# Performance work log

Hardware: AMD Instinct MI355X
Metric: run time of the kernel (lower is better)

The kernel has to match this reference:

```python
import jax, jax.numpy as jnp
import numpy as np

K = 3       # attractive nearest neighbors
J = 3       # repulsive offset (uses dist[:, :, J:])
ALPHA = 0.1
NU = 1e-3


def setup_inputs() -> dict:
    key = jax.random.key(0)
    k1, k2 = jax.random.split(key, 2)
    phi_p = jax.random.normal(k1, (4, 512, 64, 64), dtype=jnp.float32)
    memory_bank = jax.random.normal(k2, (16384, 512), dtype=jnp.float32)
    r = jnp.ones((1,), dtype=jnp.float32)
    return {"phi_p": phi_p, "memory_bank": memory_bank, "r": r}


def reference(phi_p, memory_bank, r):
    B, C, H, W = phi_p.shape
    # b c h w -> b (h w) c
    x = phi_p.reshape(B, C, H * W).transpose(0, 2, 1)
    x2 = jnp.sum(x * x, axis=-1, keepdims=True)            # [B, HW, 1]
    m2 = jnp.sum(memory_bank * memory_bank, axis=-1)       # [N]
    d2 = x2 + m2[None, None, :] - 2.0 * jnp.einsum('bnc,mc->bnm', x, memory_bank)
    d2 = jnp.maximum(d2, 0.0)                              # [B, HW, N]
    # smallest K+J squared distances, ascending (topk(largest=False))
    neg_top, _ = jax.lax.top_k(-d2, K + J)
    dist = -neg_top                                        # [B, HW, K+J]
    r2 = r ** 2
    scores_att = dist[:, :, :K] - r2
    loss_att = jnp.mean(jnp.maximum(scores_att, 0.0)) / NU
    scores_rep = r2 - dist[:, :, J:] - ALPHA
    loss_rep = jnp.mean(jnp.maximum(scores_rep, 0.0)) / NU
    return loss_att + loss_rep
```

## Files before the change

### kernel.cpp

```cpp
#include <hip/hip_runtime.h>
#include <cfloat>

#define B_   4
#define C_   512
#define HW_  4096
#define R_   16384
#define N_   16384
#define ALPHA_ 0.1f
#define SCALE_ ((float)(1000.0/49152.0))

typedef unsigned int u32;
typedef unsigned short u16;
typedef unsigned char u8;
typedef __attribute__((ext_vector_type(2))) unsigned long long u64x2;
typedef __attribute__((ext_vector_type(4))) float f32x4;

typedef const __attribute__((address_space(1))) u32* gas_u32;
typedef __attribute__((address_space(3))) u32* las_u32;

__device__ __forceinline__ void async16(const void* g, void* l) {
    __builtin_amdgcn_global_load_lds((gas_u32)g, (las_u32)l, 16, 0, 0);
}

__device__ __forceinline__ u32 pk_fp8x4(float a, float b, float c, float d) {
    u32 v = __builtin_amdgcn_cvt_pk_fp8_f32(a, b, 0, false);
    v = __builtin_amdgcn_cvt_pk_fp8_f32(c, d, v, true);
    return v;
}

__device__ __forceinline__ void ins6(float (&t)[6], float v) {
    if (v < t[5]) {
        t[5] = v;
        #pragma unroll
        for (int q = 5; q >= 1; --q) {
            float lo = fminf(t[q-1], t[q]);
            float hi = fmaxf(t[q-1], t[q]);
            t[q-1] = lo; t[q] = hi;
        }
    }
}

__global__ void conv_mem_kernel(const float* __restrict__ mem,
                                u8* __restrict__ Mb, float* __restrict__ m2) {
    int w = threadIdx.x >> 6, l = threadIdx.x & 63;
    int row = blockIdx.x * 4 + w;
    const float4* p = (const float4*)(mem + (size_t)row * C_);
    float4 a = p[l], b = p[l + 64];
    float s = a.x*a.x + a.y*a.y + a.z*a.z + a.w*a.w
            + b.x*b.x + b.y*b.y + b.z*b.z + b.w*b.w;
    *(u32*)(Mb + (size_t)row * C_ + l*4)       = pk_fp8x4(a.x, a.y, a.z, a.w);
    *(u32*)(Mb + (size_t)row * C_ + 256 + l*4) = pk_fp8x4(b.x, b.y, b.z, b.w);
    #pragma unroll
    for (int off = 32; off > 0; off >>= 1) s += __shfl_down(s, off);
    if (l == 0) m2[row] = s;
}

__global__ void conv_phi_kernel(const float* __restrict__ phi, u8* __restrict__ Xb,
                                float* __restrict__ x2) {
    __shared__ float T[64][65];
    int t = threadIdx.x;
    int n0 = blockIdx.x * 64, c0 = blockIdx.y * 64, b = blockIdx.z;
    const float* src = phi + ((size_t)b * C_ + c0) * HW_ + n0;
    int l = t & 63, cg = t >> 6;
    float sq = 0.f;
    #pragma unroll
    for (int p = 0; p < 16; ++p) {
        int c = cg + p * 4;
        float v = src[(size_t)c * HW_ + l];
        T[c][l] = v;
        sq = fmaf(v, v, sq);
    }
    atomicAdd(&x2[(size_t)b * HW_ + n0 + l], sq);
    __syncthreads();
    int cq = t & 15, gl0 = t >> 4;
    #pragma unroll
    for (int p = 0; p < 4; ++p) {
        int gl = gl0 + p * 16;
        u32 v = pk_fp8x4(T[cq*4+0][gl], T[cq*4+1][gl],
                         T[cq*4+2][gl], T[cq*4+3][gl]);
        size_t g = (size_t)b * HW_ + n0 + gl;
        *(u32*)(Xb + g * C_ + c0 + cq*4) = v;
    }
}

template<int NC>
__global__ __launch_bounds__(256, 3) void gemm_topk_kernel(
    const u8* __restrict__ Xb, const u8* __restrict__ Mb,
    const float* __restrict__ m2, float* __restrict__ P ) {
    __shared__ __align__(16) u8 smem[32768];
    const int t = threadIdx.x;
    const int w = t >> 6, l = t & 63;
    const int id   = blockIdx.x;
    const int xcd  = id & 7;
    const int cy   = (xcd * NC) >> 3;
    const int xsub = xcd - cy * (8 / NC);
    const int bx   = (id >> 3) + xsub * (256 * NC / 8);
    const int g0  = bx * 64;
    const int n0c = cy * (N_ / NC);
    const int mband = w * 32;
    const int fm  = l & 15;
    const int rq  = l >> 4;
    const int pc  = (rq ^ ((fm >> 1) & 3)) * 16;
    const int srow4 = l >> 2;
    const int soff  = (((l & 3) ^ ((l >> 3) & 3)) * 16);

    u64x2 ax[4][2];
    {
        const u8* Xr = Xb + (size_t)(g0 + w*16 + fm) * C_ + rq * 16;
        #pragma unroll
        for (int s = 0; s < 4; ++s) {
            ax[s][0] = *(const u64x2*)(Xr + s*128);
            ax[s][1] = *(const u64x2*)(Xr + s*128 + 64);
        }
    }

    float top[4][6];
    #pragma unroll
    for (int s4 = 0; s4 < 4; ++s4)
        #pragma unroll
        for (int q = 0; q < 6; ++q) top[s4][q] = FLT_MAX;

    {
        const u8* Msrc = Mb + (size_t)(n0c + mband) * C_;
        #pragma unroll
        for (int h = 0; h < 2; ++h)
            #pragma unroll
            for (int i = 0; i < 2; ++i)
                async16(Msrc + (size_t)(i*16 + srow4) * C_ + h*64 + soff,
                        smem + mband*64 + h*8192 + i*1024);
    }
    __syncthreads();

    const int NT = N_ / NC / 128;
    #pragma unroll 1
    for (int nt = 0; nt < NT; ++nt) {
        const int n0 = n0c + nt * 128;

        f32x4 acc[8];
        #pragma unroll
        for (int n = 0; n < 8; ++n) acc[n] = (f32x4)0.f;

        #pragma unroll
        for (int s = 0; s < 4; ++s) {
            {
                const int nt2 = (s == 3) ? nt + 1 : nt;
                const int s2  = (s + 1) & 3;
                if (nt2 < NT) {
                    const u8* Msrc = Mb + (size_t)(n0c + nt2*128 + mband) * C_ + s2*128;
                    u8* dst = smem + ((s+1)&1)*16384 + mband*64;
                    #pragma unroll
                    for (int h = 0; h < 2; ++h)
                        #pragma unroll
                        for (int i = 0; i < 2; ++i)
                            async16(Msrc + (size_t)(i*16 + srow4) * C_ + h*64 + soff,
                                    dst + h*8192 + i*1024);
                }
            }
            const u8* bufp = smem + (s&1)*16384;
            #pragma unroll
            for (int h = 0; h < 2; ++h) {
                const u8* Mh = bufp + h * 8192;
                const u64x2 a = ax[s][h];
                #pragma unroll
                for (int n = 0; n < 8; ++n) {
                    u64x2 bv = *(const u64x2*)(Mh + (n*16 + fm) * 64 + pc);
                    acc[n] = __builtin_amdgcn_mfma_f32_16x16x32_fp8_fp8(
                        (long)a.x, (long)bv.x, acc[n], 0, 0, 0);
                    acc[n] = __builtin_amdgcn_mfma_f32_16x16x32_fp8_fp8(
                        (long)a.y, (long)bv.y, acc[n], 0, 0, 0);
                }
            }

            if (s == 3) {
                float m2w[8];
                #pragma unroll
                for (int n = 0; n < 8; ++n) m2w[n] = m2[n0 + n * 16 + fm];
                #pragma unroll
                for (int j = 0; j < 4; ++j) {
                    float d0 = m2w[0] - 2.f * acc[0][j];
                    float d1 = m2w[1] - 2.f * acc[1][j];
                    float d2 = m2w[2] - 2.f * acc[2][j];
                    float d3 = m2w[3] - 2.f * acc[3][j];
                    float d4 = m2w[4] - 2.f * acc[4][j];
                    float d5 = m2w[5] - 2.f * acc[5][j];
                    float d6 = m2w[6] - 2.f * acc[6][j];
                    float d7 = m2w[7] - 2.f * acc[7][j];
                    float vmin = fminf(fminf(fminf(d0, d1), fminf(d2, d3)),
                                       fminf(fminf(d4, d5), fminf(d6, d7)));
                    float (&tt)[6] = top[j];
                    if (vmin < tt[5]) {
                        ins6(tt, d0); ins6(tt, d1); ins6(tt, d2); ins6(tt, d3);
                        ins6(tt, d4); ins6(tt, d5); ins6(tt, d6); ins6(tt, d7);
                    }
                }
            }
            __syncthreads();
        }
    }

    float* Mg = (float*)smem;
    #pragma unroll
    for (int j = 0; j < 4; ++j) {
        int lrow = w * 16 + rq * 4 + j;
        #pragma unroll
        for (int q = 0; q < 6; ++q)
            Mg[lrow * 97 + fm * 6 + q] = top[j][q];
    }
    __syncthreads();
    if (t < 64) {
        float t6[6];
        #pragma unroll
        for (int q = 0; q < 6; ++q) t6[q] = FLT_MAX;
        const float* row = Mg + t * 97;
        for (int v = 0; v < 96; ++v) ins6(t6, row[v]);
        float* dst = P + ((size_t)(g0 + t) * NC + cy) * 6;
        #pragma unroll
        for (int q = 0; q < 6; ++q) dst[q] = t6[q];
    }
}

template<int NC>
__global__ void finalize_kernel(const float* __restrict__ P, const float* __restrict__ x2,
                                const float* __restrict__ rp, float* __restrict__ out) {
    int g = blockIdx.x * 256 + threadIdx.x;
    float t6[6];
    #pragma unroll
    for (int q = 0; q < 6; ++q) t6[q] = FLT_MAX;
    const f32x4* pp = (const f32x4*)(P + (size_t)g * (NC * 6));
    #pragma unroll
    for (int q = 0; q < NC * 6 / 4; ++q) {
        f32x4 v = pp[q];
        ins6(t6, v.x); ins6(t6, v.y); ins6(t6, v.z); ins6(t6, v.w);
    }
    float x2g = x2[g];
    float rv = rp[0], r2 = rv * rv;
    float s = 0.f;
    #pragma unroll
    for (int i = 0; i < 3; ++i) {
        float d = fmaxf(t6[i] + x2g, 0.f);
        s += fmaxf(d - r2, 0.f);
    }
    #pragma unroll
    for (int i = 3; i < 6; ++i) {
        float d = fmaxf(t6[i] + x2g, 0.f);
        s += fmaxf(r2 - d - ALPHA_, 0.f);
    }
    #pragma unroll
    for (int off = 32; off > 0; off >>= 1) s += __shfl_down(s, off);
    __shared__ float red[4];
    int w = threadIdx.x >> 6, l = threadIdx.x & 63;
    if (l == 0) red[w] = s;
    __syncthreads();
    if (threadIdx.x == 0)
        atomicAdd(out, (red[0] + red[1] + red[2] + red[3]) * SCALE_);
}

#define TM 64
#define TN 64
#define KC 64
#define LDP 68

__global__ void m2_kernel(const float* __restrict__ mem, float* __restrict__ m2) {
    int wave = threadIdx.x >> 6, lane = threadIdx.x & 63;
    int row = blockIdx.x * 4 + wave;
    const float4* p = reinterpret_cast<const float4*>(mem + (size_t)row * C_);
    float4 a = p[lane], b = p[lane + 64];
    float s = a.x*a.x + a.y*a.y + a.z*a.z + a.w*a.w
            + b.x*b.x + b.y*b.y + b.z*b.z + b.w*b.w;
    #pragma unroll
    for (int off = 32; off > 0; off >>= 1) s += __shfl_down(s, off);
    if (lane == 0) m2[row] = s;
}

__global__ void x2f_kernel(const float* __restrict__ phi, float* __restrict__ x2) {
    int g = blockIdx.x * blockDim.x + threadIdx.x;
    int b = g >> 12;
    int n = g & 4095;
    const float* p = phi + (size_t)b * C_ * HW_ + n;
    float s = 0.f;
    #pragma unroll 8
    for (int c = 0; c < C_; ++c) {
        float v = p[(size_t)c * HW_];
        s = fmaf(v, v, s);
    }
    x2[g] = s;
}

__global__ __launch_bounds__(256) void dist_loss_kernel(
    const float* __restrict__ phi, const float* __restrict__ mem,
    const float* __restrict__ rp,  const float* __restrict__ m2,
    const float* __restrict__ x2,  float* __restrict__ out) {
    __shared__ float smem[2 * TM * LDP];
    float* xs = smem;
    float* ms = smem + TM * LDP;
    const int tid = threadIdx.x;
    const int tx = tid & 15, ty = tid >> 4;
    const int g0 = blockIdx.x * TM;
    const int b = g0 >> 12, n0img = g0 & 4095;
    const float* phiB = phi + (size_t)b * C_ * HW_ + n0img;
    float top[4][6];
    #pragma unroll
    for (int i = 0; i < 4; ++i)
        #pragma unroll
        for (int q = 0; q < 6; ++q) top[i][q] = FLT_MAX;
    float x2v[4];
    #pragma unroll
    for (int i = 0; i < 4; ++i) x2v[i] = x2[g0 + ty * 4 + i];
    for (int nt = 0; nt < N_ / TN; ++nt) {
        const int n0 = nt * TN;
        float acc[4][4];
        #pragma unroll
        for (int i = 0; i < 4; ++i)
            #pragma unroll
            for (int j = 0; j < 4; ++j) acc[i][j] = 0.f;
        for (int s = 0; s < C_ / KC; ++s) {
            const int k0 = s * KC;
            {
                int rr = tid & 63, cb = tid >> 6;
                #pragma unroll
                for (int p = 0; p < 16; ++p) {
                    int cc = p * 4 + cb;
                    xs[rr * LDP + cc] = phiB[(size_t)(k0 + cc) * HW_ + rr];
                }
            }
            {
                int kq = tid & 15, cb = tid >> 4;
                #pragma unroll
                for (int p = 0; p < 4; ++p) {
                    int c = p * 16 + cb;
                    float4 v = *reinterpret_cast<const float4*>(
                        mem + (size_t)(n0 + c) * C_ + k0 + kq * 4);
                    ms[(kq*4+0)*LDP + c] = v.x; ms[(kq*4+1)*LDP + c] = v.y;
                    ms[(kq*4+2)*LDP + c] = v.z; ms[(kq*4+3)*LDP + c] = v.w;
                }
            }
            __syncthreads();
            #pragma unroll
            for (int kq = 0; kq < KC / 4; ++kq) {
                float4 xa[4], mb[4];
                #pragma unroll
                for (int i = 0; i < 4; ++i)
                    xa[i] = *reinterpret_cast<const float4*>(&xs[(ty*4+i)*LDP + kq*4]);
                #pragma unroll
                for (int kk = 0; kk < 4; ++kk)
                    mb[kk] = *reinterpret_cast<const float4*>(&ms[(kq*4+kk)*LDP + tx*4]);
                #pragma unroll
                for (int i = 0; i < 4; ++i) {
                    const float xk[4] = {xa[i].x, xa[i].y, xa[i].z, xa[i].w};
                    #pragma unroll
                    for (int kk = 0; kk < 4; ++kk) {
                        const float mc[4] = {mb[kk].x, mb[kk].y, mb[kk].z, mb[kk].w};
                        #pragma unroll
                        for (int j = 0; j < 4; ++j)
                            acc[i][j] = fmaf(xk[kk], mc[j], acc[i][j]);
                    }
                }
            }
            __syncthreads();
        }
        #pragma unroll
        for (int j = 0; j < 4; ++j) {
            float m2v = m2[n0 + tx * 4 + j];
            #pragma unroll
            for (int i = 0; i < 4; ++i) {
                float d = fmaxf(x2v[i] + m2v - 2.f * acc[i][j], 0.f);
                ins6(top[i], d);
            }
        }
    }
    __syncthreads();
    float* mg = smem;
    #pragma unroll
    for (int i = 0; i < 4; ++i)
        #pragma unroll
        for (int q = 0; q < 6; ++q)
            mg[(ty*4+i)*97 + tx*6 + q] = top[i][q];
    __syncthreads();
    if (tid < 64) {
        float t6[6];
        #pragma unroll
        for (int q = 0; q < 6; ++q) t6[q] = FLT_MAX;
        const float* row = mg + tid * 97;
        for (int v = 0; v < 96; ++v) ins6(t6, row[v]);
        float rv = rp[0], r2 = rv * rv;
        float s = fmaxf(t6[0]-r2,0.f) + fmaxf(t6[1]-r2,0.f) + fmaxf(t6[2]-r2,0.f)
                + fmaxf(r2-t6[3]-ALPHA_,0.f) + fmaxf(r2-t6[4]-ALPHA_,0.f)
                + fmaxf(r2-t6[5]-ALPHA_,0.f);
        #pragma unroll
        for (int off = 32; off > 0; off >>= 1) s += __shfl_down(s, off);
        if (tid == 0) atomicAdd(out, s * SCALE_);
    }
}

extern "C" void kernel_launch(void* const* d_in, const int* in_sizes, int n_in,
                              void* d_out, int out_size, void* d_ws, size_t ws_size,
                              hipStream_t stream) {
    const float* phi = (const float*)d_in[0];
    const float* mem = (const float*)d_in[1];
    const float* rp  = (const float*)d_in[2];
    float* out = (float*)d_out;

    const size_t offX  = 0;
    const size_t offM  = (size_t)R_ * C_;
    const size_t offx2 = offM + (size_t)N_ * C_;
    const size_t offm2 = offx2 + (size_t)R_ * 4;
    const size_t offP  = offm2 + (size_t)N_ * 4;
    const size_t need4 = offP + (size_t)R_ * 4 * 6 * 4;

    hipMemsetAsync(out, 0, sizeof(float), stream);

    if (ws_size >= need4) {
        u8*    Xb = (u8*)((char*)d_ws + offX);
        u8*    Mb = (u8*)((char*)d_ws + offM);
        float* x2 = (float*)((char*)d_ws + offx2);
        float* m2 = (float*)((char*)d_ws + offm2);
        float* P  = (float*)((char*)d_ws + offP);

        hipMemsetAsync(x2, 0, (size_t)R_ * 4, stream);
        conv_mem_kernel<<<N_ / 4, 256, 0, stream>>>(mem, Mb, m2);
        conv_phi_kernel<<<dim3(HW_ / 64, C_ / 64, B_), 256, 0, stream>>>(phi, Xb, x2);
        gemm_topk_kernel<4><<<dim3(256 * 4, 1), 256, 0, stream>>>(Xb, Mb, m2, P);
        finalize_kernel<4><<<R_ / 256, 256, 0, stream>>>(P, x2, rp, out);
    } else {
        float* m2 = (float*)d_ws;
        float* x2 = m2 + N_;
        m2_kernel<<<N_ / 4, 256, 0, stream>>>(mem, m2);
        x2f_kernel<<<R_ / 256, 256, 0, stream>>>(phi, x2);
        dist_loss_kernel<<<R_ / TM, 256, 0, stream>>>(phi, mem, rp, m2, x2, out);
    }
}
```

Baseline: 346.2 us.

## Triple-buffer memory-bank tiles in 64-byte stages and stage m2 in LDS

Replaces the double-buffered 128-column K stages with a three-slot rotating ring of 64-column stages, prefetching two stages ahead and synchronising with a partial vmcnt wait plus a single barrier per stage. The m2 norms for the block's column range are loaded once into shared memory asynchronously instead of being read from global memory every tile. This is meant to hide global-load latency and cut barrier stalls, at the cost of more LDS per block (which may reduce occupancy) and twice as many barriers per tile. The wrap-around prefetch issues redundant loads at the end, which are drained before the final reduction.

```diff
diff --git a/kernel.cpp b/kernel.cpp
--- a/kernel.cpp
+++ b/kernel.cpp
@@ -87,7 +87,7 @@
 __global__ __launch_bounds__(256, 3) void gemm_topk_kernel(
     const u8* __restrict__ Xb, const u8* __restrict__ Mb,
     const float* __restrict__ m2, float* __restrict__ P ) {
-    __shared__ __align__(16) u8 smem[32768];
+    __shared__ __align__(16) u8 smem[40960];
     const int t = threadIdx.x;
     const int w = t >> 6, l = t & 63;
     const int id   = blockIdx.x;
@@ -120,61 +120,62 @@
         #pragma unroll
         for (int q = 0; q < 6; ++q) top[s4][q] = FLT_MAX;
 
+    float* m2s = (float*)(smem + 24576);
     {
-        const u8* Msrc = Mb + (size_t)(n0c + mband) * C_;
-        #pragma unroll
-        for (int h = 0; h < 2; ++h)
-            #pragma unroll
-            for (int i = 0; i < 2; ++i)
-                async16(Msrc + (size_t)(i*16 + srow4) * C_ + h*64 + soff,
-                        smem + mband*64 + h*8192 + i*1024);
-    }
-    __syncthreads();
-
+        const float* src = m2 + n0c + (w * 4) * 256 + l * 4;
+        u8* dst = smem + 24576 + (w * 4) * 1024;
+        #pragma unroll
+        for (int i = 0; i < 4; ++i)
+            async16(src + i * 256, dst + i * 1024);
+    }
+    {
+        #pragma unroll
+        for (int i = 0; i < 2; ++i)
+            async16(Mb + (size_t)(n0c + mband + i*16 + srow4) * C_ + 0 + soff,
+                    smem + mband*64 + i*1024);
+        #pragma unroll
+        for (int i = 0; i < 2; ++i)
+            async16(Mb + (size_t)(n0c + mband + i*16 + srow4) * C_ + 64 + soff,
+                    smem + 8192 + mband*64 + i*1024);
+    }
+
+    u8 *q0 = smem, *q1 = smem + 8192, *q2 = smem + 16384;
     const int NT = N_ / NC / 128;
     #pragma unroll 1
     for (int nt = 0; nt < NT; ++nt) {
-        const int n0 = n0c + nt * 128;
-
         f32x4 acc[8];
         #pragma unroll
         for (int n = 0; n < 8; ++n) acc[n] = (f32x4)0.f;
 
         #pragma unroll
-        for (int s = 0; s < 4; ++s) {
+        for (int ss = 0; ss < 8; ++ss) {
+            asm volatile("s_waitcnt vmcnt(2)" ::: "memory");
+            __builtin_amdgcn_s_barrier();
             {
-                const int nt2 = (s == 3) ? nt + 1 : nt;
-                const int s2  = (s + 1) & 3;
-                if (nt2 < NT) {
-                    const u8* Msrc = Mb + (size_t)(n0c + nt2*128 + mband) * C_ + s2*128;
-                    u8* dst = smem + ((s+1)&1)*16384 + mband*64;
-                    #pragma unroll
-                    for (int h = 0; h < 2; ++h)
-                        #pragma unroll
-                        for (int i = 0; i < 2; ++i)
-                            async16(Msrc + (size_t)(i*16 + srow4) * C_ + h*64 + soff,
-                                    dst + h*8192 + i*1024);
-                }
-            }
-            const u8* bufp = smem + (s&1)*16384;
-            #pragma unroll
-            for (int h = 0; h < 2; ++h) {
-                const u8* Mh = bufp + h * 8192;
-                const u64x2 a = ax[s][h];
+                int g2 = nt * 8 + ss + 2;
+                if (g2 >= NT * 8) g2 -= NT * 8;
+                const int nt2 = g2 >> 3, ss2 = g2 & 7;
+                const u8* Msrc = Mb + (size_t)(n0c + nt2*128 + mband) * C_ + ss2*64;
+                #pragma unroll
+                for (int i = 0; i < 2; ++i)
+                    async16(Msrc + (size_t)(i*16 + srow4) * C_ + soff,
+                            q2 + mband*64 + i*1024);
+            }
+            {
+                const u64x2 a = ax[ss >> 1][ss & 1];
                 #pragma unroll
                 for (int n = 0; n < 8; ++n) {
-                    u64x2 bv = *(const u64x2*)(Mh + (n*16 + fm) * 64 + pc);
+                    u64x2 bv = *(const u64x2*)(q0 + (n*16 + fm) * 64 + pc);
                     acc[n] = __builtin_amdgcn_mfma_f32_16x16x32_fp8_fp8(
                         (long)a.x, (long)bv.x, acc[n], 0, 0, 0);
                     acc[n] = __builtin_amdgcn_mfma_f32_16x16x32_fp8_fp8(
                         (long)a.y, (long)bv.y, acc[n], 0, 0, 0);
                 }
             }
-
-            if (s == 3) {
+            if (ss == 7) {
                 float m2w[8];
                 #pragma unroll
-                for (int n = 0; n < 8; ++n) m2w[n] = m2[n0 + n * 16 + fm];
+                for (int n = 0; n < 8; ++n) m2w[n] = m2s[nt*128 + n*16 + fm];
                 #pragma unroll
                 for (int j = 0; j < 4; ++j) {
                     float d0 = m2w[0] - 2.f * acc[0][j];
@@ -194,9 +195,12 @@
                     }
                 }
             }
-            __syncthreads();
+            u8* tq = q0; q0 = q1; q1 = q2; q2 = tq;
         }
     }
+
+    asm volatile("s_waitcnt vmcnt(0)" ::: "memory");
+    __syncthreads();
 
     float* Mg = (float*)smem;
     #pragma unroll
```

After: 346.2 us. Within noise of the previous version (+0.0%).

## Pre-swizzle memory bank into fragment layout and load half of B directly to registers

Applied to the files above, without the earlier changes.

The fp8 memory bank is now written in a tiled fragment-order layout, so each lane's MFMA operand is a contiguous 16-byte chunk. The GEMM kernel stages only half of each 128-column N tile through LDS and loads the other half straight from global memory into registers. This roughly halves LDS traffic and LDS footprint per block, and drops the XOR swizzle arithmetic. In exchange it adds global-load latency inside the inner loop and more register pressure under the 3-blocks-per-SM launch bound.

```diff
diff --git a/kernel.cpp b/kernel.cpp
--- a/kernel.cpp
+++ b/kernel.cpp
@@ -48,8 +48,11 @@
     float4 a = p[l], b = p[l + 64];
     float s = a.x*a.x + a.y*a.y + a.z*a.z + a.w*a.w
             + b.x*b.x + b.y*b.y + b.z*b.z + b.w*b.w;
-    *(u32*)(Mb + (size_t)row * C_ + l*4)       = pk_fp8x4(a.x, a.y, a.z, a.w);
-    *(u32*)(Mb + (size_t)row * C_ + 256 + l*4) = pk_fp8x4(b.x, b.y, b.z, b.w);
+    u8* base = Mb + (size_t)(row >> 4) * 8192;
+    int fm = row & 15;
+    int h1 = l >> 4, rqb = ((l >> 2) & 3) * 256 + (l & 3) * 4;
+    *(u32*)(base + h1*1024       + fm*16 + rqb) = pk_fp8x4(a.x, a.y, a.z, a.w);
+    *(u32*)(base + (4+h1)*1024   + fm*16 + rqb) = pk_fp8x4(b.x, b.y, b.z, b.w);
     #pragma unroll
     for (int off = 32; off > 0; off >>= 1) s += __shfl_down(s, off);
     if (l == 0) m2[row] = s;
@@ -87,7 +90,7 @@
 __global__ __launch_bounds__(256, 3) void gemm_topk_kernel(
     const u8* __restrict__ Xb, const u8* __restrict__ Mb,
     const float* __restrict__ m2, float* __restrict__ P ) {
-    __shared__ __align__(16) u8 smem[32768];
+    __shared__ __align__(16) u8 smem[24832];
     const int t = threadIdx.x;
     const int w = t >> 6, l = t & 63;
     const int id   = blockIdx.x;
@@ -97,12 +100,8 @@
     const int bx   = (id >> 3) + xsub * (256 * NC / 8);
     const int g0  = bx * 64;
     const int n0c = cy * (N_ / NC);
-    const int mband = w * 32;
     const int fm  = l & 15;
     const int rq  = l >> 4;
-    const int pc  = (rq ^ ((fm >> 1) & 3)) * 16;
-    const int srow4 = l >> 2;
-    const int soff  = (((l & 3) ^ ((l >> 3) & 3)) * 16);
 
     u64x2 ax[4][2];
     {
@@ -120,21 +119,20 @@
         #pragma unroll
         for (int q = 0; q < 6; ++q) top[s4][q] = FLT_MAX;
 
+    const int n0t0 = n0c >> 4;
     {
-        const u8* Msrc = Mb + (size_t)(n0c + mband) * C_;
-        #pragma unroll
-        for (int h = 0; h < 2; ++h)
-            #pragma unroll
-            for (int i = 0; i < 2; ++i)
-                async16(Msrc + (size_t)(i*16 + srow4) * C_ + h*64 + soff,
-                        smem + mband*64 + h*8192 + i*1024);
+        #pragma unroll
+        for (int i = 0; i < 2; ++i)
+            async16(Mb + ((size_t)(n0t0 + i*2 + (w>>1))*8 + (w&1))*1024 + l*16,
+                    smem + i*4096 + w*1024);
     }
     __syncthreads();
 
     const int NT = N_ / NC / 128;
     #pragma unroll 1
     for (int nt = 0; nt < NT; ++nt) {
-        const int n0 = n0c + nt * 128;
+        const int n0  = n0c + nt * 128;
+        const int n0t = n0t0 + nt * 8;
 
         f32x4 acc[8];
         #pragma unroll
@@ -142,32 +140,48 @@
 
         #pragma unroll
         for (int s = 0; s < 4; ++s) {
+            u64x2 bd[8];
+            #pragma unroll
+            for (int np = 0; np < 4; ++np)
+                #pragma unroll
+                for (int kh = 0; kh < 2; ++kh)
+                    bd[np*2+kh] = *(const u64x2*)(
+                        Mb + ((size_t)(n0t + 4 + np)*8 + 2*s + kh)*1024 + l*16);
             {
                 const int nt2 = (s == 3) ? nt + 1 : nt;
                 const int s2  = (s + 1) & 3;
                 if (nt2 < NT) {
-                    const u8* Msrc = Mb + (size_t)(n0c + nt2*128 + mband) * C_ + s2*128;
-                    u8* dst = smem + ((s+1)&1)*16384 + mband*64;
+                    const int n0t2 = n0t0 + nt2 * 8;
+                    u8* dst = smem + ((s+1)&1)*8192;
                     #pragma unroll
-                    for (int h = 0; h < 2; ++h)
-                        #pragma unroll
-                        for (int i = 0; i < 2; ++i)
-                            async16(Msrc + (size_t)(i*16 + srow4) * C_ + h*64 + soff,
-                                    dst + h*8192 + i*1024);
-                }
-            }
-            const u8* bufp = smem + (s&1)*16384;
-            #pragma unroll
-            for (int h = 0; h < 2; ++h) {
-                const u8* Mh = bufp + h * 8192;
-                const u64x2 a = ax[s][h];
-                #pragma unroll
-                for (int n = 0; n < 8; ++n) {
-                    u64x2 bv = *(const u64x2*)(Mh + (n*16 + fm) * 64 + pc);
+                    for (int i = 0; i < 2; ++i)
+                        async16(Mb + ((size_t)(n0t2 + i*2 + (w>>1))*8
+                                      + 2*s2 + (w&1))*1024 + l*16,
+                                dst + i*4096 + w*1024);
+                }
+            }
+            const u8* bufp = smem + (s&1)*8192;
+            #pragma unroll
+            for (int kh = 0; kh < 2; ++kh) {
+                const u64x2 a = ax[s][kh];
+                #pragma unroll
+                for (int n = 0; n < 4; ++n) {
+                    u64x2 bv = *(const u64x2*)(bufp + (n*2 + kh)*1024 + l*16);
                     acc[n] = __builtin_amdgcn_mfma_f32_16x16x32_fp8_fp8(
                         (long)a.x, (long)bv.x, acc[n], 0, 0, 0);
                     acc[n] = __builtin_amdgcn_mfma_f32_16x16x32_fp8_fp8(
                         (long)a.y, (long)bv.y, acc[n], 0, 0, 0);
+                }
+            }
+            #pragma unroll
+            for (int kh = 0; kh < 2; ++kh) {
+                const u64x2 a = ax[s][kh];
+                #pragma unroll
+                for (int np = 0; np < 4; ++np) {
+                    acc[4+np] = __builtin_amdgcn_mfma_f32_16x16x32_fp8_fp8(
+                        (long)a.x, (long)bd[np*2+kh].x, acc[4+np], 0, 0, 0);
+                    acc[4+np] = __builtin_amdgcn_mfma_f32_16x16x32_fp8_fp8(
+                        (long)a.y, (long)bd[np*2+kh].y, acc[4+np], 0, 0, 0);
                 }
             }
 
```

New measurement: 485.7 us. +40.3%, slower.

## Use 32x32 fp8 MFMA with MFMA-native pre-swizzled layouts and 8-way N split

Applied to the files above, without the earlier changes.

Converts both X and memory bank to a pre-tiled fp8 layout matching the 32x32x16 MFMA operand order, so tiles load with contiguous 16-byte accesses and no LDS swizzle. The GEMM switches from 16x16x32 to 32x32x16 MFMA, with each wave owning 32 query rows. X operands are now streamed from global memory per k-step instead of held in registers. The N dimension is split into 8 chunks when workspace allows, giving more blocks and halving LDS use. The trade-off is more global X traffic and a larger partial top-k buffer for the finalize step.

```diff
diff --git a/kernel.cpp b/kernel.cpp
--- a/kernel.cpp
+++ b/kernel.cpp
@@ -14,6 +14,7 @@
 typedef unsigned char u8;
 typedef __attribute__((ext_vector_type(2))) unsigned long long u64x2;
 typedef __attribute__((ext_vector_type(4))) float f32x4;
+typedef __attribute__((ext_vector_type(16))) float f32x16;
 
 typedef const __attribute__((address_space(1))) u32* gas_u32;
 typedef __attribute__((address_space(3))) u32* las_u32;
@@ -39,6 +40,7 @@
         }
     }
 }
+
 
 __global__ void conv_mem_kernel(const float* __restrict__ mem,
                                 u8* __restrict__ Mb, float* __restrict__ m2) {
@@ -48,8 +50,18 @@
     float4 a = p[l], b = p[l + 64];
     float s = a.x*a.x + a.y*a.y + a.z*a.z + a.w*a.w
             + b.x*b.x + b.y*b.y + b.z*b.z + b.w*b.w;
-    *(u32*)(Mb + (size_t)row * C_ + l*4)       = pk_fp8x4(a.x, a.y, a.z, a.w);
-    *(u32*)(Mb + (size_t)row * C_ + 256 + l*4) = pk_fp8x4(b.x, b.y, b.z, b.w);
+    u8* base = Mb + (size_t)(row >> 5) * 16384;
+    int r31 = row & 31;
+    {
+        int kb = 4 * l;
+        *(u32*)(base + ((kb>>4)>>1)*1024 + ((((kb>>3)&1)<<5) + r31)*16
+                + ((kb>>4)&1)*8 + (kb&4)) = pk_fp8x4(a.x, a.y, a.z, a.w);
+    }
+    {
+        int kb = 256 + 4 * l;
+        *(u32*)(base + ((kb>>4)>>1)*1024 + ((((kb>>3)&1)<<5) + r31)*16
+                + ((kb>>4)&1)*8 + (kb&4)) = pk_fp8x4(b.x, b.y, b.z, b.w);
+    }
     #pragma unroll
     for (int off = 32; off > 0; off >>= 1) s += __shfl_down(s, off);
     if (l == 0) m2[row] = s;
@@ -78,8 +90,10 @@
         int gl = gl0 + p * 16;
         u32 v = pk_fp8x4(T[cq*4+0][gl], T[cq*4+1][gl],
                          T[cq*4+2][gl], T[cq*4+3][gl]);
-        size_t g = (size_t)b * HW_ + n0 + gl;
-        *(u32*)(Xb + g * C_ + c0 + cq*4) = v;
+        int g = (int)((size_t)b * HW_ + n0 + gl);
+        int kb = c0 + cq * 4;
+        *(u32*)(Xb + (size_t)(g >> 5) * 16384 + ((kb>>4)>>1)*1024
+                + ((((kb>>3)&1)<<5) + (g & 31))*16 + ((kb>>4)&1)*8 + (kb&4)) = v;
     }
 }
 
@@ -87,110 +101,90 @@
 __global__ __launch_bounds__(256, 3) void gemm_topk_kernel(
     const u8* __restrict__ Xb, const u8* __restrict__ Mb,
     const float* __restrict__ m2, float* __restrict__ P ) {
-    __shared__ __align__(16) u8 smem[32768];
+    __shared__ __align__(16) u8 smem[16384];
     const int t = threadIdx.x;
     const int w = t >> 6, l = t & 63;
     const int id   = blockIdx.x;
     const int xcd  = id & 7;
     const int cy   = (xcd * NC) >> 3;
     const int xsub = xcd - cy * (8 / NC);
-    const int bx   = (id >> 3) + xsub * (256 * NC / 8);
-    const int g0  = bx * 64;
-    const int n0c = cy * (N_ / NC);
-    const int mband = w * 32;
-    const int fm  = l & 15;
-    const int rq  = l >> 4;
-    const int pc  = (rq ^ ((fm >> 1) & 3)) * 16;
-    const int srow4 = l >> 2;
-    const int soff  = (((l & 3) ^ ((l >> 3) & 3)) * 16);
-
-    u64x2 ax[4][2];
+    const int bx   = (id >> 3) + xsub * (128 * NC / 8);
+    const int g0   = bx * 128;
+    const int n0c  = cy * (N_ / NC);
+    const int n32c = n0c >> 5;
+    const int xt   = (g0 >> 5) + w;
+    const int col  = l & 31, h = l >> 5;
+
+    float top[6];
+    #pragma unroll
+    for (int q = 0; q < 6; ++q) top[q] = FLT_MAX;
+
     {
-        const u8* Xr = Xb + (size_t)(g0 + w*16 + fm) * C_ + rq * 16;
-        #pragma unroll
-        for (int s = 0; s < 4; ++s) {
-            ax[s][0] = *(const u64x2*)(Xr + s*128);
-            ax[s][1] = *(const u64x2*)(Xr + s*128 + 64);
-        }
-    }
-
-    float top[4][6];
-    #pragma unroll
-    for (int s4 = 0; s4 < 4; ++s4)
-        #pragma unroll
-        for (int q = 0; q < 6; ++q) top[s4][q] = FLT_MAX;
-
-    {
-        const u8* Msrc = Mb + (size_t)(n0c + mband) * C_;
-        #pragma unroll
-        for (int h = 0; h < 2; ++h)
-            #pragma unroll
-            for (int i = 0; i < 2; ++i)
-                async16(Msrc + (size_t)(i*16 + srow4) * C_ + h*64 + soff,
-                        smem + mband*64 + h*8192 + i*1024);
+        const u8* Msrc = Mb + (size_t)(n32c + w) * 16384;
+        #pragma unroll
+        for (int pp = 0; pp < 2; ++pp)
+            async16(Msrc + pp*1024 + l*16, smem + w*2048 + pp*1024);
     }
     __syncthreads();
 
     const int NT = N_ / NC / 128;
     #pragma unroll 1
     for (int nt = 0; nt < NT; ++nt) {
-        const int n0 = n0c + nt * 128;
-
-        f32x4 acc[8];
-        #pragma unroll
-        for (int n = 0; n < 8; ++n) acc[n] = (f32x4)0.f;
-
-        #pragma unroll
-        for (int s = 0; s < 4; ++s) {
+        f32x16 acc[4];
+        #pragma unroll
+        for (int n = 0; n < 4; ++n) acc[n] = (f32x16)0.f;
+
+        #pragma unroll
+        for (int s = 0; s < 8; ++s) {
+            const int cur = (nt * 8 + s) & 1;
+            u64x2 xv0 = *(const u64x2*)(Xb + ((size_t)xt*16 + 2*s  )*1024 + l*16);
+            u64x2 xv1 = *(const u64x2*)(Xb + ((size_t)xt*16 + 2*s+1)*1024 + l*16);
             {
-                const int nt2 = (s == 3) ? nt + 1 : nt;
-                const int s2  = (s + 1) & 3;
-                if (nt2 < NT) {
-                    const u8* Msrc = Mb + (size_t)(n0c + nt2*128 + mband) * C_ + s2*128;
-                    u8* dst = smem + ((s+1)&1)*16384 + mband*64;
+                const int gs2 = nt * 8 + s + 1;
+                if (gs2 < NT * 8) {
+                    const int nt2 = gs2 >> 3, s2 = gs2 & 7;
+                    const u8* Msrc = Mb + (size_t)(n32c + nt2*4 + w) * 16384
+                                        + (size_t)(2*s2) * 1024;
+                    u8* dst = smem + (cur^1)*8192 + w*2048;
                     #pragma unroll
-                    for (int h = 0; h < 2; ++h)
+                    for (int pp = 0; pp < 2; ++pp)
+                        async16(Msrc + pp*1024 + l*16, dst + pp*1024);
+                }
+            }
+            const u8* buf = smem + cur*8192;
+            #pragma unroll
+            for (int pp = 0; pp < 2; ++pp) {
+                const u64x2 xv = pp ? xv1 : xv0;
+                #pragma unroll
+                for (int tt = 0; tt < 4; ++tt) {
+                    u64x2 bm = *(const u64x2*)(buf + tt*2048 + pp*1024 + l*16);
+                    acc[tt] = __builtin_amdgcn_mfma_f32_32x32x16_fp8_fp8(
+                        (long)bm.x, (long)xv.x, acc[tt], 0, 0, 0);
+                    acc[tt] = __builtin_amdgcn_mfma_f32_32x32x16_fp8_fp8(
+                        (long)bm.y, (long)xv.y, acc[tt], 0, 0, 0);
+                }
+            }
+
+            if (s == 7) {
+                const int n0 = n0c + nt * 128;
+                #pragma unroll
+                for (int tt = 0; tt < 4; ++tt) {
+                    const f32x4* m2p = (const f32x4*)(m2 + n0 + tt*32 + h*4);
+                    float dv[16];
+                    float vmin = FLT_MAX;
+                    #pragma unroll
+                    for (int gq = 0; gq < 4; ++gq) {
+                        f32x4 mv = m2p[gq * 2];
                         #pragma unroll
-                        for (int i = 0; i < 2; ++i)
-                            async16(Msrc + (size_t)(i*16 + srow4) * C_ + h*64 + soff,
-                                    dst + h*8192 + i*1024);
-                }
-            }
-            const u8* bufp = smem + (s&1)*16384;
-            #pragma unroll
-            for (int h = 0; h < 2; ++h) {
-                const u8* Mh = bufp + h * 8192;
-                const u64x2 a = ax[s][h];
-                #pragma unroll
-                for (int n = 0; n < 8; ++n) {
-                    u64x2 bv = *(const u64x2*)(Mh + (n*16 + fm) * 64 + pc);
-                    acc[n] = __builtin_amdgcn_mfma_f32_16x16x32_fp8_fp8(
-                        (long)a.x, (long)bv.x, acc[n], 0, 0, 0);
-                    acc[n] = __builtin_amdgcn_mfma_f32_16x16x32_fp8_fp8(
-                        (long)a.y, (long)bv.y, acc[n], 0, 0, 0);
-                }
-            }
-
-            if (s == 3) {
-                float m2w[8];
-                #pragma unroll
-                for (int n = 0; n < 8; ++n) m2w[n] = m2[n0 + n * 16 + fm];
-                #pragma unroll
-                for (int j = 0; j < 4; ++j) {
-                    float d0 = m2w[0] - 2.f * acc[0][j];
-                    float d1 = m2w[1] - 2.f * acc[1][j];
-                    float d2 = m2w[2] - 2.f * acc[2][j];
-                    float d3 = m2w[3] - 2.f * acc[3][j];
-                    float d4 = m2w[4] - 2.f * acc[4][j];
-                    float d5 = m2w[5] - 2.f * acc[5][j];
-                    float d6 = m2w[6] - 2.f * acc[6][j];
-                    float d7 = m2w[7] - 2.f * acc[7][j];
-                    float vmin = fminf(fminf(fminf(d0, d1), fminf(d2, d3)),
-                                       fminf(fminf(d4, d5), fminf(d6, d7)));
-                    float (&tt)[6] = top[j];
-                    if (vmin < tt[5]) {
-                        ins6(tt, d0); ins6(tt, d1); ins6(tt, d2); ins6(tt, d3);
-                        ins6(tt, d4); ins6(tt, d5); ins6(tt, d6); ins6(tt, d7);
+                        for (int c = 0; c < 4; ++c) {
+                            float d = mv[c] - 2.f * acc[tt][gq*4 + c];
+                            dv[gq*4 + c] = d;
+                            vmin = fminf(vmin, d);
+                        }
+                    }
+                    if (vmin < top[5]) {
+                        #pragma unroll
+                        for (int i = 0; i < 16; ++i) ins6(top, dv[i]);
                     }
                 }
             }
@@ -199,20 +193,20 @@
     }
 
     float* Mg = (float*)smem;
-    #pragma unroll
-    for (int j = 0; j < 4; ++j) {
-        int lrow = w * 16 + rq * 4 + j;
+    {
+        int lrow = w * 32 + col;
         #pragma unroll
         for (int q = 0; q < 6; ++q)
-            Mg[lrow * 97 + fm * 6 + q] = top[j][q];
-    }
-    __syncthreads();
-    if (t < 64) {
+            Mg[lrow * 13 + h * 6 + q] = top[q];
+    }
+    __syncthreads();
+    if (t < 128) {
         float t6[6];
         #pragma unroll
         for (int q = 0; q < 6; ++q) t6[q] = FLT_MAX;
-        const float* row = Mg + t * 97;
-        for (int v = 0; v < 96; ++v) ins6(t6, row[v]);
+        const float* row = Mg + t * 13;
+        #pragma unroll
+        for (int v = 0; v < 12; ++v) ins6(t6, row[v]);
         float* dst = P + ((size_t)(g0 + t) * NC + cy) * 6;
         #pragma unroll
         for (int q = 0; q < 6; ++q) dst[q] = t6[q];
@@ -405,6 +399,7 @@
     const size_t offx2 = offM + (size_t)N_ * C_;
     const size_t offm2 = offx2 + (size_t)R_ * 4;
     const size_t offP  = offm2 + (size_t)N_ * 4;
+    const size_t need8 = offP + (size_t)R_ * 8 * 6 * 4;
     const size_t need4 = offP + (size_t)R_ * 4 * 6 * 4;
 
     hipMemsetAsync(out, 0, sizeof(float), stream);
@@ -419,8 +414,13 @@
         hipMemsetAsync(x2, 0, (size_t)R_ * 4, stream);
         conv_mem_kernel<<<N_ / 4, 256, 0, stream>>>(mem, Mb, m2);
         conv_phi_kernel<<<dim3(HW_ / 64, C_ / 64, B_), 256, 0, stream>>>(phi, Xb, x2);
-        gemm_topk_kernel<4><<<dim3(256 * 4, 1), 256, 0, stream>>>(Xb, Mb, m2, P);
-        finalize_kernel<4><<<R_ / 256, 256, 0, stream>>>(P, x2, rp, out);
+        if (ws_size >= need8) {
+            gemm_topk_kernel<8><<<dim3(128 * 8, 1), 256, 0, stream>>>(Xb, Mb, m2, P);
+            finalize_kernel<8><<<R_ / 256, 256, 0, stream>>>(P, x2, rp, out);
+        } else {
+            gemm_topk_kernel<4><<<dim3(128 * 4, 1), 256, 0, stream>>>(Xb, Mb, m2, P);
+            finalize_kernel<4><<<R_ / 256, 256, 0, stream>>>(P, x2, rp, out);
+        }
     } else {
         float* m2 = (float*)d_ws;
         float* x2 = m2 + N_;
```

Result: no change. 342.4 us (-1.1%).
